# Optimization experiments

Measured on AMD Instinct MI355X. Metric: run time of the kernel, lower is better.

## Reference

```python
import jax, jax.numpy as jnp
import numpy as np

N_NODES = 100000
N_EDGES = 1600000
IN_DIM = 128
OUT_DIM = 128
LEAKY_SLOPE = 0.01  # torch nn.LeakyReLU default


def setup_inputs() -> dict:
    key = jax.random.key(0)
    k1, k2, k3, k4 = jax.random.split(key, 4)
    x = jax.random.normal(k1, (N_NODES, IN_DIM), dtype=jnp.float32)
    edge_index = jax.random.randint(k2, (2, N_EDGES), 0, N_NODES, dtype=jnp.int64)
    edge_attr = jax.random.uniform(k3, (N_EDGES,), dtype=jnp.float32)
    # Linear params (xavier_uniform weight, zero bias)
    limit = np.sqrt(6.0 / (IN_DIM + OUT_DIM)).astype(np.float32)
    W = jax.random.uniform(k4, (OUT_DIM, IN_DIM), minval=-limit, maxval=limit, dtype=jnp.float32)
    b = jnp.zeros((OUT_DIM,), dtype=jnp.float32)
    return {"x": x, "edge_index": edge_index, "edge_attr": edge_attr, "W": W, "b": b}


def reference(x, edge_index, edge_attr, W, b):
    src = edge_index[0]  # x_j (source nodes)
    dst = edge_index[1]  # aggregation index (target nodes)
    # message: gather source features, scale by per-edge scalar  [E, D]
    msg = x[src] * edge_attr[:, None]
    # aggregate: scatter-add over target index  [N, D]
    agg = jax.ops.segment_sum(msg, dst, num_segments=N_NODES)
    # update: Linear + LeakyReLU (dropout is identity at p=0 / eval)
    out = agg @ W.T + b
    return jnp.where(out >= 0, out, LEAKY_SLOPE * out)
```

## Files before the change

kernel.cpp:

```cpp
#include <hip/hip_runtime.h>

#define N_NODES 100000
#define N_EDGES 1600000
#define DIM 128
#define LEAKY 0.01f
#define RS_STRIDE 132
#define WS_STRIDE 132
#define NBUCKET 391
#define SB_EDGES 4096
#define NSB 391

typedef short bf16x8 __attribute__((ext_vector_type(8)));
typedef float f32x4 __attribute__((ext_vector_type(4)));

static __device__ __forceinline__ unsigned short f2bf(float f) {
  unsigned int u = __float_as_uint(f);
  u = (u + 0x7fffu + ((u >> 16) & 1u)) >> 16;
  return (unsigned short)u;
}

__global__ __launch_bounds__(512) void sort_local_kernel(
    const int* __restrict__ ei, const float* __restrict__ attr,
    int2* __restrict__ binned, unsigned short* __restrict__ counts,
    int* __restrict__ srcOff, const float4* __restrict__ x4,
    ushort4* __restrict__ xb4) {
  __shared__ int hist[NBUCKET];
  __shared__ int cursor[NBUCKET];
  __shared__ int scanBuf[512];
  __shared__ int2 stage[SB_EDGES];

  const int t = threadIdx.x;
  const int blk = blockIdx.x;
  const int base = blk * SB_EDGES;
  const int n = min(SB_EDGES, N_EDGES - base);

  if (t < NBUCKET) hist[t] = 0;
  __syncthreads();

  int myP[8];
  int myB[8];
  float myA[8];
#pragma unroll
  for (int k = 0; k < 8; ++k) {
    int i = t + k * 512;
    if (i < n) {
      int e = base + i;
      int s = ei[e];
      int d = ei[N_EDGES + e];
      myA[k] = attr[e];
      myB[k] = d >> 8;
      myP[k] = s | ((d & 255) << 17);
      atomicAdd(&hist[myB[k]], 1);
    } else {
      myB[k] = -1;
    }
  }
  __syncthreads();

  int v = (t < NBUCKET) ? hist[t] : 0;
  scanBuf[t] = v;
  __syncthreads();
  for (int off = 1; off < 512; off <<= 1) {
    int u = (t >= off) ? scanBuf[t - off] : 0;
    __syncthreads();
    scanBuf[t] += u;
    __syncthreads();
  }
  if (t < NBUCKET) {
    int excl = scanBuf[t] - v;
    cursor[t] = excl;
    counts[(size_t)t * NSB + blk] = (unsigned short)v;
    srcOff[(size_t)t * NSB + blk] = base + excl;
  }
  __syncthreads();

#pragma unroll
  for (int k = 0; k < 8; ++k) {
    if (myB[k] >= 0) {
      int loc = atomicAdd(&cursor[myB[k]], 1);
      stage[loc] = make_int2(myP[k], __float_as_int(myA[k]));
    }
  }
  __syncthreads();

  for (int i = t; i < n; i += 512) binned[base + i] = stage[i];

  if (xb4) {
    for (int i = blk * 512 + t; i < (N_NODES * DIM) / 4; i += NSB * 512) {
      float4 vv = x4[i];
      ushort4 o;
      o.x = f2bf(vv.x); o.y = f2bf(vv.y); o.z = f2bf(vv.z); o.w = f2bf(vv.w);
      xb4[i] = o;
    }
  }
}

__global__ __launch_bounds__(128) void bucket_count_kernel(
    const unsigned short* __restrict__ counts, int* __restrict__ bucketCount) {
  __shared__ int red[128];
  const int b = blockIdx.x;
  const int t = threadIdx.x;
  int s = 0;
  for (int sb = t; sb < NSB; sb += 128) s += counts[(size_t)b * NSB + sb];
  red[t] = s;
  __syncthreads();
  for (int off = 64; off > 0; off >>= 1) {
    if (t < off) red[t] += red[t + off];
    __syncthreads();
  }
  if (t == 0) bucketCount[b] = red[0];
}

__global__ __launch_bounds__(512) void bucket_scan_kernel(
    const int* __restrict__ bucketCount, int* __restrict__ bucketBase) {
  __shared__ int s[512];
  const int t = threadIdx.x;
  int v = (t < NBUCKET) ? bucketCount[t] : 0;
  s[t] = v;
  __syncthreads();
  for (int off = 1; off < 512; off <<= 1) {
    int u = (t >= off) ? s[t - off] : 0;
    __syncthreads();
    s[t] += u;
    __syncthreads();
  }
  if (t < NBUCKET) bucketBase[t] = s[t] - v;
}

__global__ __launch_bounds__(448) void passB_kernel(
    const int2* __restrict__ binned, const unsigned short* __restrict__ counts,
    const int* __restrict__ srcOff, const int* __restrict__ bucketBase,
    int2* __restrict__ csr, int* __restrict__ row_ptr) {
  __shared__ int runSrc[NSB];
  __shared__ int runLen[NSB];
  __shared__ int hist[256];
  __shared__ int cur[256];
  __shared__ int scanBuf[256];

  const int b = blockIdx.x;
  const int t = threadIdx.x;

  if (t < NSB) {
    runSrc[t] = srcOff[(size_t)b * NSB + t];
    runLen[t] = (int)counts[(size_t)b * NSB + t];
  }
  if (t < 256) hist[t] = 0;
  __syncthreads();

  if (t < NSB) {
    const int src = runSrc[t];
    const int len = runLen[t];
    for (int j = 0; j < len; ++j) {
      int px = binned[src + j].x;
      atomicAdd(&hist[(px >> 17) & 255], 1);
    }
  }
  __syncthreads();

  int hv = (t < 256) ? hist[t] : 0;
  if (t < 256) scanBuf[t] = hv;
  __syncthreads();
  for (int off = 1; off < 256; off <<= 1) {
    int u = 0;
    if (t < 256 && t >= off) u = scanBuf[t - off];
    __syncthreads();
    if (t < 256) scanBuf[t] += u;
    __syncthreads();
  }
  const int bb = bucketBase[b];
  if (t < 256) {
    int excl = scanBuf[t] - hv;
    cur[t] = excl;
    int node = b * 256 + t;
    if (node < N_NODES) row_ptr[node] = bb + excl;
  }
  if (b == 0 && t == 0) row_ptr[N_NODES] = N_EDGES;
  __syncthreads();

  if (t < NSB) {
    const int src = runSrc[t];
    const int len = runLen[t];
    for (int j = 0; j < len; ++j) {
      int2 rec = binned[src + j];
      int ld = (rec.x >> 17) & 255;
      int pos = bb + atomicAdd(&cur[ld], 1);
      csr[pos] = make_int2(rec.x & 0x1FFFF, rec.y);
    }
  }
}

__global__ __launch_bounds__(256) void gather_aggb_kernel(
    const unsigned short* __restrict__ xb, const int* __restrict__ row_ptr,
    const int2* __restrict__ csr, unsigned int* __restrict__ aggB) {
  const int node = blockIdx.x * 4 + (threadIdx.x >> 6);
  const int lane = threadIdx.x & 63;

  const int beg = row_ptr[node];
  const int end = row_ptr[node + 1];

  float2 acc = make_float2(0.f, 0.f);
  int e = beg;
  for (; e + 3 < end; e += 4) {
    int2 e0 = csr[e];
    int2 e1 = csr[e + 1];
    int2 e2 = csr[e + 2];
    int2 e3 = csr[e + 3];
    unsigned int u0 = *(const unsigned int*)(xb + (size_t)e0.x * DIM + lane * 2);
    unsigned int u1 = *(const unsigned int*)(xb + (size_t)e1.x * DIM + lane * 2);
    unsigned int u2 = *(const unsigned int*)(xb + (size_t)e2.x * DIM + lane * 2);
    unsigned int u3 = *(const unsigned int*)(xb + (size_t)e3.x * DIM + lane * 2);
    float a0 = __int_as_float(e0.y), a1 = __int_as_float(e1.y);
    float a2 = __int_as_float(e2.y), a3 = __int_as_float(e3.y);
    acc.x += __uint_as_float(u0 << 16) * a0;
    acc.y += __uint_as_float(u0 & 0xffff0000u) * a0;
    acc.x += __uint_as_float(u1 << 16) * a1;
    acc.y += __uint_as_float(u1 & 0xffff0000u) * a1;
    acc.x += __uint_as_float(u2 << 16) * a2;
    acc.y += __uint_as_float(u2 & 0xffff0000u) * a2;
    acc.x += __uint_as_float(u3 << 16) * a3;
    acc.y += __uint_as_float(u3 & 0xffff0000u) * a3;
  }
  for (; e < end; ++e) {
    int2 e0 = csr[e];
    float a0 = __int_as_float(e0.y);
    unsigned int u0 = *(const unsigned int*)(xb + (size_t)e0.x * DIM + lane * 2);
    acc.x += __uint_as_float(u0 << 16) * a0;
    acc.y += __uint_as_float(u0 & 0xffff0000u) * a0;
  }
  aggB[(size_t)node * 64 + lane] =
      (unsigned int)f2bf(acc.x) | ((unsigned int)f2bf(acc.y) << 16);
}

__global__ __launch_bounds__(256) void gather_bf16_kernel(
    const unsigned short* __restrict__ xb, const int* __restrict__ row_ptr,
    const int2* __restrict__ csr, float* __restrict__ out) {
  const int node = blockIdx.x * 4 + (threadIdx.x >> 6);
  const int lane = threadIdx.x & 63;

  const int beg = row_ptr[node];
  const int end = row_ptr[node + 1];

  float2 acc = make_float2(0.f, 0.f);
  int e = beg;
  for (; e + 3 < end; e += 4) {
    int2 e0 = csr[e];
    int2 e1 = csr[e + 1];
    int2 e2 = csr[e + 2];
    int2 e3 = csr[e + 3];
    unsigned int u0 = *(const unsigned int*)(xb + (size_t)e0.x * DIM + lane * 2);
    unsigned int u1 = *(const unsigned int*)(xb + (size_t)e1.x * DIM + lane * 2);
    unsigned int u2 = *(const unsigned int*)(xb + (size_t)e2.x * DIM + lane * 2);
    unsigned int u3 = *(const unsigned int*)(xb + (size_t)e3.x * DIM + lane * 2);
    float a0 = __int_as_float(e0.y), a1 = __int_as_float(e1.y);
    float a2 = __int_as_float(e2.y), a3 = __int_as_float(e3.y);
    acc.x += __uint_as_float(u0 << 16) * a0;
    acc.y += __uint_as_float(u0 & 0xffff0000u) * a0;
    acc.x += __uint_as_float(u1 << 16) * a1;
    acc.y += __uint_as_float(u1 & 0xffff0000u) * a1;
    acc.x += __uint_as_float(u2 << 16) * a2;
    acc.y += __uint_as_float(u2 & 0xffff0000u) * a2;
    acc.x += __uint_as_float(u3 << 16) * a3;
    acc.y += __uint_as_float(u3 & 0xffff0000u) * a3;
  }
  for (; e < end; ++e) {
    int2 e0 = csr[e];
    float a0 = __int_as_float(e0.y);
    unsigned int u0 = *(const unsigned int*)(xb + (size_t)e0.x * DIM + lane * 2);
    acc.x += __uint_as_float(u0 << 16) * a0;
    acc.y += __uint_as_float(u0 & 0xffff0000u) * a0;
  }
  *(float2*)(out + (size_t)node * DIM + lane * 2) = acc;
}

__global__ __launch_bounds__(256) void gather_f32_kernel(
    const float* __restrict__ x, const int* __restrict__ row_ptr,
    const int2* __restrict__ csr, float* __restrict__ out) {
  const int node = blockIdx.x * 4 + (threadIdx.x >> 6);
  const int lane = threadIdx.x & 63;

  const int beg = row_ptr[node];
  const int end = row_ptr[node + 1];

  float2 acc = make_float2(0.f, 0.f);
  int e = beg;
  for (; e + 3 < end; e += 4) {
    int2 e0 = csr[e];
    int2 e1 = csr[e + 1];
    int2 e2 = csr[e + 2];
    int2 e3 = csr[e + 3];
    float2 v0 = *(const float2*)(x + (size_t)e0.x * DIM + lane * 2);
    float2 v1 = *(const float2*)(x + (size_t)e1.x * DIM + lane * 2);
    float2 v2 = *(const float2*)(x + (size_t)e2.x * DIM + lane * 2);
    float2 v3 = *(const float2*)(x + (size_t)e3.x * DIM + lane * 2);
    float a0 = __int_as_float(e0.y), a1 = __int_as_float(e1.y);
    float a2 = __int_as_float(e2.y), a3 = __int_as_float(e3.y);
    acc.x += v0.x * a0; acc.y += v0.y * a0;
    acc.x += v1.x * a1; acc.y += v1.y * a1;
    acc.x += v2.x * a2; acc.y += v2.y * a2;
    acc.x += v3.x * a3; acc.y += v3.y * a3;
  }
  for (; e < end; ++e) {
    int2 e0 = csr[e];
    float a0 = __int_as_float(e0.y);
    float2 v0 = *(const float2*)(x + (size_t)e0.x * DIM + lane * 2);
    acc.x += v0.x * a0; acc.y += v0.y * a0;
  }
  *(float2*)(out + (size_t)node * DIM + lane * 2) = acc;
}

__global__ __launch_bounds__(256) void w_frag_kernel(
    const float* __restrict__ W, bf16x8* __restrict__ wfrag) {
  const int gid = blockIdx.x * 256 + threadIdx.x;
  const int lane = gid & 63;
  const int q = (gid >> 6) & 3;
  const int nt = gid >> 8;
  const int n = nt * 16 + (lane & 15);
  const int kb = q * 32 + ((lane >> 4) & 3) * 8;
  const float4 f0 = *(const float4*)(W + n * DIM + kb);
  const float4 f1 = *(const float4*)(W + n * DIM + kb + 4);
  bf16x8 frag;
  frag[0] = (short)f2bf(f0.x); frag[1] = (short)f2bf(f0.y);
  frag[2] = (short)f2bf(f0.z); frag[3] = (short)f2bf(f0.w);
  frag[4] = (short)f2bf(f1.x); frag[5] = (short)f2bf(f1.y);
  frag[6] = (short)f2bf(f1.z); frag[7] = (short)f2bf(f1.w);
  wfrag[gid] = frag;
}

__global__ __launch_bounds__(256) void linear_mfma_bf16_kernel(
    const unsigned short* __restrict__ aggB, const bf16x8* __restrict__ wfrag,
    const float* __restrict__ bias, float* __restrict__ out) {
  const int wave = threadIdx.x >> 6;
  const int lane = threadIdx.x & 63;
  const int r0 = (blockIdx.x * 4 + wave) * 16;
  if (r0 >= N_NODES) return;

  const int m = lane & 15;
  const int quad = lane >> 4;
  const int row = r0 + m;

  bf16x8 afrag[4];
#pragma unroll
  for (int q = 0; q < 4; ++q) {
    afrag[q] = *(const bf16x8*)(aggB + (size_t)row * DIM + q * 32 + quad * 8);
  }

#pragma unroll
  for (int nt = 0; nt < 8; ++nt) {
    const float bv = bias[nt * 16 + m];
    f32x4 acc = {bv, bv, bv, bv};
#pragma unroll
    for (int q = 0; q < 4; ++q) {
      bf16x8 bfrag = wfrag[(nt * 4 + q) * 64 + lane];
      acc = __builtin_amdgcn_mfma_f32_16x16x32_bf16(afrag[q], bfrag, acc, 0, 0, 0);
    }
    const int col = nt * 16 + m;
#pragma unroll
    for (int i = 0; i < 4; ++i) {
      float v = acc[i];
      v = v >= 0.f ? v : v * LEAKY;
      out[(size_t)(r0 + quad * 4 + i) * DIM + col] = v;
    }
  }
}

__global__ __launch_bounds__(256) void linear_mfma_kernel(
    const float* __restrict__ agg, const bf16x8* __restrict__ wfrag,
    const float* __restrict__ bias, float* __restrict__ out) {
  const int wave = threadIdx.x >> 6;
  const int lane = threadIdx.x & 63;
  const int r0 = (blockIdx.x * 4 + wave) * 16;
  if (r0 >= N_NODES) return;

  const int m = lane & 15;
  const int quad = lane >> 4;
  const int row = r0 + m;

  bf16x8 afrag[4];
#pragma unroll
  for (int q = 0; q < 4; ++q) {
    const float* ap = agg + (size_t)row * DIM + q * 32 + quad * 8;
    const float4 f0 = *(const float4*)(ap);
    const float4 f1 = *(const float4*)(ap + 4);
    afrag[q][0] = (short)f2bf(f0.x); afrag[q][1] = (short)f2bf(f0.y);
    afrag[q][2] = (short)f2bf(f0.z); afrag[q][3] = (short)f2bf(f0.w);
    afrag[q][4] = (short)f2bf(f1.x); afrag[q][5] = (short)f2bf(f1.y);
    afrag[q][6] = (short)f2bf(f1.z); afrag[q][7] = (short)f2bf(f1.w);
  }

#pragma unroll
  for (int nt = 0; nt < 8; ++nt) {
    const float bv = bias[nt * 16 + m];
    f32x4 acc = {bv, bv, bv, bv};
#pragma unroll
    for (int q = 0; q < 4; ++q) {
      bf16x8 bfrag = wfrag[(nt * 4 + q) * 64 + lane];
      acc = __builtin_amdgcn_mfma_f32_16x16x32_bf16(afrag[q], bfrag, acc, 0, 0, 0);
    }
    const int col = nt * 16 + m;
#pragma unroll
    for (int i = 0; i < 4; ++i) {
      float v = acc[i];
      v = v >= 0.f ? v : v * LEAKY;
      out[(size_t)(r0 + quad * 4 + i) * DIM + col] = v;
    }
  }
}

__global__ __launch_bounds__(256) void x2b_kernel(
    const float4* __restrict__ x, ushort4* __restrict__ xb) {
  const int i = blockIdx.x * 256 + threadIdx.x;
  float4 v = x[i];
  ushort4 o;
  o.x = f2bf(v.x); o.y = f2bf(v.y); o.z = f2bf(v.z); o.w = f2bf(v.w);
  xb[i] = o;
}

__global__ __launch_bounds__(256) void scatter_kernel(
    const float* __restrict__ x, const int* __restrict__ ei,
    const float* __restrict__ attr, float* __restrict__ agg) {
  int gid = blockIdx.x * blockDim.x + threadIdx.x;
  int e = gid >> 5;
  int f = (gid & 31) * 4;
  if (e >= N_EDGES) return;
  int s = ei[e];
  int d = ei[N_EDGES + e];
  float a = attr[e];
  const float4 xv = *(const float4*)(x + (size_t)s * DIM + f);
  float* dp = agg + (size_t)d * DIM + f;
  atomicAdd(dp + 0, xv.x * a);
  atomicAdd(dp + 1, xv.y * a);
  atomicAdd(dp + 2, xv.z * a);
  atomicAdd(dp + 3, xv.w * a);
}

__global__ __launch_bounds__(256, 2) void linear_kernel(
    const float* __restrict__ agg, const float* __restrict__ W,
    const float* __restrict__ bias, float* __restrict__ out) {
  __shared__ float Rs[32 * RS_STRIDE];
  __shared__ float Ws[64 * WS_STRIDE];

  const int tid = threadIdx.x;
  const int c = (tid & 31) * 4;
  const int rg = tid >> 5;
  const size_t rowBase = (size_t)blockIdx.x * 32;

  {
    const int lr = tid >> 3;
    const int col = (tid & 7) * 16;
    const float4* src = (const float4*)(agg + (rowBase + lr) * DIM + col);
#pragma unroll
    for (int j = 0; j < 4; ++j) {
      *(float4*)(Rs + lr * RS_STRIDE + col + j * 4) = src[j];
    }
  }

  const float4 bv = *(const float4*)(bias + c);
  float4 acc0 = bv, acc1 = bv, acc2 = bv, acc3 = bv;

  for (int half = 0; half < 2; ++half) {
    __syncthreads();
    {
      const int k0 = tid >> 7;
      const int o = tid & 127;
#pragma unroll
      for (int kk = k0; kk < 64; kk += 2) {
        Ws[kk * WS_STRIDE + o] = W[o * DIM + half * 64 + kk];
      }
    }
    __syncthreads();

    const float* rs0 = Rs + (rg * 4 + 0) * RS_STRIDE + half * 64;
    const float* rs1 = Rs + (rg * 4 + 1) * RS_STRIDE + half * 64;
    const float* rs2 = Rs + (rg * 4 + 2) * RS_STRIDE + half * 64;
    const float* rs3 = Rs + (rg * 4 + 3) * RS_STRIDE + half * 64;

#pragma unroll 8
    for (int k4 = 0; k4 < 16; ++k4) {
      const float4 v0 = *(const float4*)(rs0 + k4 * 4);
      const float4 v1 = *(const float4*)(rs1 + k4 * 4);
      const float4 v2 = *(const float4*)(rs2 + k4 * 4);
      const float4 v3 = *(const float4*)(rs3 + k4 * 4);
      const float4 w0 = *(const float4*)(Ws + (k4 * 4 + 0) * WS_STRIDE + c);
      const float4 w1 = *(const float4*)(Ws + (k4 * 4 + 1) * WS_STRIDE + c);
      const float4 w2 = *(const float4*)(Ws + (k4 * 4 + 2) * WS_STRIDE + c);
      const float4 w3 = *(const float4*)(Ws + (k4 * 4 + 3) * WS_STRIDE + c);

#define FMA4(acc, v)                                               \
      acc.x += v.x * w0.x + v.y * w1.x + v.z * w2.x + v.w * w3.x;  \
      acc.y += v.x * w0.y + v.y * w1.y + v.z * w2.y + v.w * w3.y;  \
      acc.z += v.x * w0.z + v.y * w1.z + v.z * w2.z + v.w * w3.z;  \
      acc.w += v.x * w0.w + v.y * w1.w + v.z * w2.w + v.w * w3.w;
      FMA4(acc0, v0)
      FMA4(acc1, v1)
      FMA4(acc2, v2)
      FMA4(acc3, v3)
#undef FMA4
    }
  }

#define LEAKY4(acc)                                   \
  acc.x = acc.x >= 0.f ? acc.x : acc.x * LEAKY;       \
  acc.y = acc.y >= 0.f ? acc.y : acc.y * LEAKY;       \
  acc.z = acc.z >= 0.f ? acc.z : acc.z * LEAKY;       \
  acc.w = acc.w >= 0.f ? acc.w : acc.w * LEAKY;
  LEAKY4(acc0) LEAKY4(acc1) LEAKY4(acc2) LEAKY4(acc3)
#undef LEAKY4

  const int row0 = (int)rowBase + rg * 4;
  *(float4*)(out + (size_t)(row0 + 0) * DIM + c) = acc0;
  *(float4*)(out + (size_t)(row0 + 1) * DIM + c) = acc1;
  *(float4*)(out + (size_t)(row0 + 2) * DIM + c) = acc2;
  *(float4*)(out + (size_t)(row0 + 3) * DIM + c) = acc3;
}

extern "C" void kernel_launch(void* const* d_in, const int* in_sizes, int n_in,
                              void* d_out, int out_size, void* d_ws, size_t ws_size,
                              hipStream_t stream) {
  const float* x = (const float*)d_in[0];
  const int* ei = (const int*)d_in[1];
  const float* attr = (const float*)d_in[2];
  const float* W = (const float*)d_in[3];
  const float* b = (const float*)d_in[4];
  float* out = (float*)d_out;

  const size_t offBinned = 0;
  const size_t offCounts = 12812288;
  const size_t offSrcOff = offCounts + 305920;
  const size_t offBCount = offSrcOff + 611584;
  const size_t offBBase  = offBCount + 1792;
  const size_t offCsr    = offBBase + 1792;
  const size_t offRowPtr = offCsr + 12812288;
  const size_t offWfrag  = offRowPtr + 400128;
  const size_t sortNeed  = offWfrag + 32768;
  const size_t offXb     = sortNeed;
  const size_t fullNeed  = offXb + 25600000;
  const size_t offAggB   = fullNeed;
  const size_t bf16Need  = offAggB + 25600000;

  if (ws_size >= sortNeed) {
    char* ws = (char*)d_ws;
    int2* binned = (int2*)(ws + offBinned);
    unsigned short* counts = (unsigned short*)(ws + offCounts);
    int* srcOff = (int*)(ws + offSrcOff);
    int* bucketCount = (int*)(ws + offBCount);
    int* bucketBase = (int*)(ws + offBBase);
    int2* csr = (int2*)(ws + offCsr);
    int* row_ptr = (int*)(ws + offRowPtr);
    bf16x8* wfrag = (bf16x8*)(ws + offWfrag);
    const bool haveXb = ws_size >= fullNeed;
    const bool haveAggB = ws_size >= bf16Need;
    unsigned short* xb = haveXb ? (unsigned short*)(ws + offXb) : nullptr;
    unsigned int* aggB = haveAggB ? (unsigned int*)(ws + offAggB) : nullptr;

    w_frag_kernel<<<8, 256, 0, stream>>>(W, wfrag);
    sort_local_kernel<<<NSB, 512, 0, stream>>>(ei, attr, binned, counts, srcOff,
                                               (const float4*)x, (ushort4*)xb);
    bucket_count_kernel<<<NBUCKET, 128, 0, stream>>>(counts, bucketCount);
    bucket_scan_kernel<<<1, 512, 0, stream>>>(bucketCount, bucketBase);
    passB_kernel<<<NBUCKET, 448, 0, stream>>>(binned, counts, srcOff, bucketBase,
                                              csr, row_ptr);
    if (haveAggB) {
      gather_aggb_kernel<<<N_NODES / 4, 256, 0, stream>>>(xb, row_ptr, csr, aggB);
      linear_mfma_bf16_kernel<<<(N_NODES + 63) / 64, 256, 0, stream>>>(
          (const unsigned short*)aggB, wfrag, b, out);
    } else if (haveXb) {
      gather_bf16_kernel<<<N_NODES / 4, 256, 0, stream>>>(xb, row_ptr, csr, out);
      linear_mfma_kernel<<<(N_NODES + 63) / 64, 256, 0, stream>>>(out, wfrag, b, out);
    } else {
      gather_f32_kernel<<<N_NODES / 4, 256, 0, stream>>>(x, row_ptr, csr, out);
      linear_mfma_kernel<<<(N_NODES + 63) / 64, 256, 0, stream>>>(out, wfrag, b, out);
    }
  } else {
    hipMemsetAsync(out, 0, (size_t)N_NODES * DIM * sizeof(float), stream);
    scatter_kernel<<<(N_EDGES * 32) / 256, 256, 0, stream>>>(x, ei, attr, out);
    linear_kernel<<<N_NODES / 32, 256, 0, stream>>>(out, W, b, out);
  }
}
```

Baseline: 249.5 us.

## Fold W-fragment and x-to-bf16 conversion into bucket count; gather two nodes per wave

Removes the separate w_frag kernel launch by adding 16 extra blocks to bucket_count that build the bf16 MFMA weight fragments. The x-to-bf16 conversion moves out of sort_local into bucket_count, spread over all blocks of that launch. The gather kernel now processes two destination nodes per wavefront with interleaved 6-edge batches, raising memory-level parallelism for the random row loads. The trade-offs are higher register pressure in the gather and a heavier bucket_count kernel.

```diff
diff --git a/kernel.cpp b/kernel.cpp
--- a/kernel.cpp
+++ b/kernel.cpp
@@ -22,8 +22,7 @@
 __global__ __launch_bounds__(512) void sort_local_kernel(
     const int* __restrict__ ei, const float* __restrict__ attr,
     int2* __restrict__ binned, unsigned short* __restrict__ counts,
-    int* __restrict__ srcOff, const float4* __restrict__ x4,
-    ushort4* __restrict__ xb4) {
+    int* __restrict__ srcOff) {
   __shared__ int hist[NBUCKET];
   __shared__ int cursor[NBUCKET];
   __shared__ int scanBuf[512];
@@ -84,31 +83,52 @@
   __syncthreads();
 
   for (int i = t; i < n; i += 512) binned[base + i] = stage[i];
+}
+
+__global__ __launch_bounds__(128) void bucket_count_kernel(
+    const unsigned short* __restrict__ counts, int* __restrict__ bucketCount,
+    const float* __restrict__ W, bf16x8* __restrict__ wfrag,
+    const float4* __restrict__ x4, ushort4* __restrict__ xb4) {
+  __shared__ int red[128];
+  const int b = blockIdx.x;
+  const int t = threadIdx.x;
+
+  if (b < NBUCKET) {
+    int s = 0;
+    for (int sb = t; sb < NSB; sb += 128) s += counts[(size_t)b * NSB + sb];
+    red[t] = s;
+    __syncthreads();
+    for (int off = 64; off > 0; off >>= 1) {
+      if (t < off) red[t] += red[t + off];
+      __syncthreads();
+    }
+    if (t == 0) bucketCount[b] = red[0];
+  } else {
+    const int gid = (b - NBUCKET) * 128 + t;
+    const int lane = gid & 63;
+    const int q = (gid >> 6) & 3;
+    const int nt = gid >> 8;
+    const int n = nt * 16 + (lane & 15);
+    const int kb = q * 32 + ((lane >> 4) & 3) * 8;
+    const float4 f0 = *(const float4*)(W + n * DIM + kb);
+    const float4 f1 = *(const float4*)(W + n * DIM + kb + 4);
+    bf16x8 frag;
+    frag[0] = (short)f2bf(f0.x); frag[1] = (short)f2bf(f0.y);
+    frag[2] = (short)f2bf(f0.z); frag[3] = (short)f2bf(f0.w);
+    frag[4] = (short)f2bf(f1.x); frag[5] = (short)f2bf(f1.y);
+    frag[6] = (short)f2bf(f1.z); frag[7] = (short)f2bf(f1.w);
+    wfrag[gid] = frag;
+  }
 
   if (xb4) {
-    for (int i = blk * 512 + t; i < (N_NODES * DIM) / 4; i += NSB * 512) {
+    const int stride = (NBUCKET + 16) * 128;
+    for (int i = b * 128 + t; i < (N_NODES * DIM) / 4; i += stride) {
       float4 vv = x4[i];
       ushort4 o;
       o.x = f2bf(vv.x); o.y = f2bf(vv.y); o.z = f2bf(vv.z); o.w = f2bf(vv.w);
       xb4[i] = o;
     }
   }
-}
-
-__global__ __launch_bounds__(128) void bucket_count_kernel(
-    const unsigned short* __restrict__ counts, int* __restrict__ bucketCount) {
-  __shared__ int red[128];
-  const int b = blockIdx.x;
-  const int t = threadIdx.x;
-  int s = 0;
-  for (int sb = t; sb < NSB; sb += 128) s += counts[(size_t)b * NSB + sb];
-  red[t] = s;
-  __syncthreads();
-  for (int off = 64; off > 0; off >>= 1) {
-    if (t < off) red[t] += red[t + off];
-    __syncthreads();
-  }
-  if (t == 0) bucketCount[b] = red[0];
 }
 
 __global__ __launch_bounds__(512) void bucket_scan_kernel(
@@ -192,6 +212,100 @@
 __global__ __launch_bounds__(256) void gather_aggb_kernel(
     const unsigned short* __restrict__ xb, const int* __restrict__ row_ptr,
     const int2* __restrict__ csr, unsigned int* __restrict__ aggB) {
+  const int w = threadIdx.x >> 6;
+  const int lane = threadIdx.x & 63;
+  const int nA = blockIdx.x * 8 + w * 2;
+  const int nB = nA + 1;
+
+  int a = row_ptr[nA];
+  const int aEnd = row_ptr[nA + 1];
+  int b = row_ptr[nB];
+  const int bEnd = row_ptr[nB + 1];
+
+  float2 accA = make_float2(0.f, 0.f);
+  float2 accB = make_float2(0.f, 0.f);
+
+  while (a + 5 < aEnd && b + 5 < bEnd) {
+    int2 ea[6], eb[6];
+#pragma unroll
+    for (int k = 0; k < 6; ++k) {
+      ea[k] = csr[a + k];
+      eb[k] = csr[b + k];
+    }
+    unsigned int ua[6], ub[6];
+#pragma unroll
+    for (int k = 0; k < 6; ++k) {
+      ua[k] = *(const unsigned int*)(xb + (size_t)ea[k].x * DIM + lane * 2);
+      ub[k] = *(const unsigned int*)(xb + (size_t)eb[k].x * DIM + lane * 2);
+    }
+#pragma unroll
+    for (int k = 0; k < 6; ++k) {
+      float fa = __int_as_float(ea[k].y);
+      float fb = __int_as_float(eb[k].y);
+      accA.x += __uint_as_float(ua[k] << 16) * fa;
+      accA.y += __uint_as_float(ua[k] & 0xffff0000u) * fa;
+      accB.x += __uint_as_float(ub[k] << 16) * fb;
+      accB.y += __uint_as_float(ub[k] & 0xffff0000u) * fb;
+    }
+    a += 6;
+    b += 6;
+  }
+
+  for (; a + 3 < aEnd; a += 4) {
+    int2 e[4];
+#pragma unroll
+    for (int k = 0; k < 4; ++k) e[k] = csr[a + k];
+    unsigned int u[4];
+#pragma unroll
+    for (int k = 0; k < 4; ++k)
+      u[k] = *(const unsigned int*)(xb + (size_t)e[k].x * DIM + lane * 2);
+#pragma unroll
+    for (int k = 0; k < 4; ++k) {
+      float f = __int_as_float(e[k].y);
+      accA.x += __uint_as_float(u[k] << 16) * f;
+      accA.y += __uint_as_float(u[k] & 0xffff0000u) * f;
+    }
+  }
+  for (; a < aEnd; ++a) {
+    int2 e0 = csr[a];
+    float f0 = __int_as_float(e0.y);
+    unsigned int u0 = *(const unsigned int*)(xb + (size_t)e0.x * DIM + lane * 2);
+    accA.x += __uint_as_float(u0 << 16) * f0;
+    accA.y += __uint_as_float(u0 & 0xffff0000u) * f0;
+  }
+
+  for (; b + 3 < bEnd; b += 4) {
+    int2 e[4];
+#pragma unroll
+    for (int k = 0; k < 4; ++k) e[k] = csr[b + k];
+    unsigned int u[4];
+#pragma unroll
+    for (int k = 0; k < 4; ++k)
+      u[k] = *(const unsigned int*)(xb + (size_t)e[k].x * DIM + lane * 2);
+#pragma unroll
+    for (int k = 0; k < 4; ++k) {
+      float f = __int_as_float(e[k].y);
+      accB.x += __uint_as_float(u[k] << 16) * f;
+      accB.y += __uint_as_float(u[k] & 0xffff0000u) * f;
+    }
+  }
+  for (; b < bEnd; ++b) {
+    int2 e0 = csr[b];
+    float f0 = __int_as_float(e0.y);
+    unsigned int u0 = *(const unsigned int*)(xb + (size_t)e0.x * DIM + lane * 2);
+    accB.x += __uint_as_float(u0 << 16) * f0;
+    accB.y += __uint_as_float(u0 & 0xffff0000u) * f0;
+  }
+
+  aggB[(size_t)nA * 64 + lane] =
+      (unsigned int)f2bf(accA.x) | ((unsigned int)f2bf(accA.y) << 16);
+  aggB[(size_t)nB * 64 + lane] =
+      (unsigned int)f2bf(accB.x) | ((unsigned int)f2bf(accB.y) << 16);
+}
+
+__global__ __launch_bounds__(256) void gather_bf16_kernel(
+    const unsigned short* __restrict__ xb, const int* __restrict__ row_ptr,
+    const int2* __restrict__ csr, float* __restrict__ out) {
   const int node = blockIdx.x * 4 + (threadIdx.x >> 6);
   const int lane = threadIdx.x & 63;
 
@@ -227,48 +341,6 @@
     acc.x += __uint_as_float(u0 << 16) * a0;
     acc.y += __uint_as_float(u0 & 0xffff0000u) * a0;
   }
-  aggB[(size_t)node * 64 + lane] =
-      (unsigned int)f2bf(acc.x) | ((unsigned int)f2bf(acc.y) << 16);
-}
-
-__global__ __launch_bounds__(256) void gather_bf16_kernel(
-    const unsigned short* __restrict__ xb, const int* __restrict__ row_ptr,
-    const int2* __restrict__ csr, float* __restrict__ out) {
-  const int node = blockIdx.x * 4 + (threadIdx.x >> 6);
-  const int lane = threadIdx.x & 63;
-
-  const int beg = row_ptr[node];
-  const int end = row_ptr[node + 1];
-
-  float2 acc = make_float2(0.f, 0.f);
-  int e = beg;
-  for (; e + 3 < end; e += 4) {
-    int2 e0 = csr[e];
-    int2 e1 = csr[e + 1];
-    int2 e2 = csr[e + 2];
-    int2 e3 = csr[e + 3];
-    unsigned int u0 = *(const unsigned int*)(xb + (size_t)e0.x * DIM + lane * 2);
-    unsigned int u1 = *(const unsigned int*)(xb + (size_t)e1.x * DIM + lane * 2);
-    unsigned int u2 = *(const unsigned int*)(xb + (size_t)e2.x * DIM + lane * 2);
-    unsigned int u3 = *(const unsigned int*)(xb + (size_t)e3.x * DIM + lane * 2);
-    float a0 = __int_as_float(e0.y), a1 = __int_as_float(e1.y);
-    float a2 = __int_as_float(e2.y), a3 = __int_as_float(e3.y);
-    acc.x += __uint_as_float(u0 << 16) * a0;
-    acc.y += __uint_as_float(u0 & 0xffff0000u) * a0;
-    acc.x += __uint_as_float(u1 << 16) * a1;
-    acc.y += __uint_as_float(u1 & 0xffff0000u) * a1;
-    acc.x += __uint_as_float(u2 << 16) * a2;
-    acc.y += __uint_as_float(u2 & 0xffff0000u) * a2;
-    acc.x += __uint_as_float(u3 << 16) * a3;
-    acc.y += __uint_as_float(u3 & 0xffff0000u) * a3;
-  }
-  for (; e < end; ++e) {
-    int2 e0 = csr[e];
-    float a0 = __int_as_float(e0.y);
-    unsigned int u0 = *(const unsigned int*)(xb + (size_t)e0.x * DIM + lane * 2);
-    acc.x += __uint_as_float(u0 << 16) * a0;
-    acc.y += __uint_as_float(u0 & 0xffff0000u) * a0;
-  }
   *(float2*)(out + (size_t)node * DIM + lane * 2) = acc;
 }
 
@@ -308,24 +380,6 @@
   *(float2*)(out + (size_t)node * DIM + lane * 2) = acc;
 }
 
-__global__ __launch_bounds__(256) void w_frag_kernel(
-    const float* __restrict__ W, bf16x8* __restrict__ wfrag) {
-  const int gid = blockIdx.x * 256 + threadIdx.x;
-  const int lane = gid & 63;
-  const int q = (gid >> 6) & 3;
-  const int nt = gid >> 8;
-  const int n = nt * 16 + (lane & 15);
-  const int kb = q * 32 + ((lane >> 4) & 3) * 8;
-  const float4 f0 = *(const float4*)(W + n * DIM + kb);
-  const float4 f1 = *(const float4*)(W + n * DIM + kb + 4);
-  bf16x8 frag;
-  frag[0] = (short)f2bf(f0.x); frag[1] = (short)f2bf(f0.y);
-  frag[2] = (short)f2bf(f0.z); frag[3] = (short)f2bf(f0.w);
-  frag[4] = (short)f2bf(f1.x); frag[5] = (short)f2bf(f1.y);
-  frag[6] = (short)f2bf(f1.z); frag[7] = (short)f2bf(f1.w);
-  wfrag[gid] = frag;
-}
-
 __global__ __launch_bounds__(256) void linear_mfma_bf16_kernel(
     const unsigned short* __restrict__ aggB, const bf16x8* __restrict__ wfrag,
     const float* __restrict__ bias, float* __restrict__ out) {
@@ -404,15 +458,6 @@
       out[(size_t)(r0 + quad * 4 + i) * DIM + col] = v;
     }
   }
-}
-
-__global__ __launch_bounds__(256) void x2b_kernel(
-    const float4* __restrict__ x, ushort4* __restrict__ xb) {
-  const int i = blockIdx.x * 256 + threadIdx.x;
-  float4 v = x[i];
-  ushort4 o;
-  o.x = f2bf(v.x); o.y = f2bf(v.y); o.z = f2bf(v.z); o.w = f2bf(v.w);
-  xb[i] = o;
 }
 
 __global__ __launch_bounds__(256) void scatter_kernel(
@@ -552,15 +597,14 @@
     unsigned short* xb = haveXb ? (unsigned short*)(ws + offXb) : nullptr;
     unsigned int* aggB = haveAggB ? (unsigned int*)(ws + offAggB) : nullptr;
 
-    w_frag_kernel<<<8, 256, 0, stream>>>(W, wfrag);
-    sort_local_kernel<<<NSB, 512, 0, stream>>>(ei, attr, binned, counts, srcOff,
-                                               (const float4*)x, (ushort4*)xb);
-    bucket_count_kernel<<<NBUCKET, 128, 0, stream>>>(counts, bucketCount);
+    sort_local_kernel<<<NSB, 512, 0, stream>>>(ei, attr, binned, counts, srcOff);
+    bucket_count_kernel<<<NBUCKET + 16, 128, 0, stream>>>(
+        counts, bucketCount, W, wfrag, (const float4*)x, (ushort4*)xb);
     bucket_scan_kernel<<<1, 512, 0, stream>>>(bucketCount, bucketBase);
     passB_kernel<<<NBUCKET, 448, 0, stream>>>(binned, counts, srcOff, bucketBase,
                                               csr, row_ptr);
     if (haveAggB) {
-      gather_aggb_kernel<<<N_NODES / 4, 256, 0, stream>>>(xb, row_ptr, csr, aggB);
+      gather_aggb_kernel<<<N_NODES / 8, 256, 0, stream>>>(xb, row_ptr, csr, aggB);
       linear_mfma_bf16_kernel<<<(N_NODES + 63) / 64, 256, 0, stream>>>(
           (const unsigned short*)aggB, wfrag, b, out);
     } else if (haveXb) {
```

After: 246.8 us. Within noise of the previous version (-1.1%).
